# Kernel optimization log

Hardware: AMD Instinct MI355X
Metric: run time of the kernel (lower is better)

Reference implementation:

```python
import jax, jax.numpy as jnp
import numpy as np

T, B, C = 1024, 16, 1024
H, K, PAD_L = 16, 7, 3  # num_heads, kernel_size, padding_l
OUT = 1024


def setup_inputs() -> dict:
    key = jax.random.key(0)
    ks = jax.random.split(key, 8)
    s_in = 1.0 / np.sqrt(C)
    return {
        "x": jax.random.normal(ks[0], (T, B, C), dtype=jnp.float32),
        "W1": jax.random.normal(ks[1], (C, C), dtype=jnp.float32) * s_in,
        "b1": jnp.zeros((C,), dtype=jnp.float32),
        "Wq": jax.random.normal(ks[2], (C, H * K), dtype=jnp.float32) * s_in,
        "bq": jnp.zeros((H * K,), dtype=jnp.float32),
        "conv_bias": jax.random.normal(ks[3], (C,), dtype=jnp.float32) * 0.02,
        "W2": jax.random.normal(ks[4], (C, OUT), dtype=jnp.float32) * s_in,
        "b2": jnp.zeros((OUT,), dtype=jnp.float32),
    }


def reference(x, W1, b1, Wq, bq, conv_bias, W2, b2):
    # linear1 (glu=False -> no activation)
    h = x @ W1 + b1                       # [T, B, C]
    Tn, Bn, Cn = h.shape
    R = Cn // H                           # channels per head
    # dynamic filter prediction from query (= h), softmax over K taps
    w = (h @ Wq + bq).reshape(Tn, Bn, H, K)
    w = jax.nn.softmax(w, axis=-1)        # [T, B, H, K]
    # unfold1d: pad PAD_L left, K-1-PAD_L right along time, gather K-windows
    hp = jnp.pad(h, ((PAD_L, K - 1 - PAD_L), (0, 0), (0, 0)))
    win = jnp.stack([hp[k:k + Tn] for k in range(K)], axis=-1)  # [T, B, C, K]
    win = win.reshape(Tn, Bn, H, R, K)
    out = jnp.einsum('tbhrk,tbhk->tbhr', win, w).reshape(Tn, Bn, Cn)
    out = out + conv_bias                 # [T, B, C]
    return out @ W2 + b2                  # [T, B, OUT]
```

## Files before the change

kernel.cpp:

```cpp
#include <hip/hip_runtime.h>
#include <math.h>

#define T_DIM 1024
#define B_DIM 16
#define C_DIM 1024
#define H_DIM 16
#define K_TAPS 7
#define PAD_LEFT 3
#define OUT_DIM 1024
#define M_DIM (T_DIM * B_DIM)
#define HK 112
#define HKP 128
#define KD 1024
#define NT (KD / 64)

typedef __attribute__((ext_vector_type(8))) short bf16x8;
typedef __attribute__((ext_vector_type(4))) float f32x4;

__device__ __forceinline__ ushort f2bf(float f) {
    union { float f; unsigned u; } v; v.f = f;
    unsigned u = v.u;
    u += 0x7fffu + ((u >> 16) & 1u);
    return (ushort)(u >> 16);
}
__device__ __forceinline__ float bf2f(ushort h) {
    union { unsigned u; float f; } v; v.u = ((unsigned)h) << 16;
    return v.f;
}

__global__ __launch_bounds__(256) void cvt_bf16x8(const float* __restrict__ in,
                                                  ushort* __restrict__ out,
                                                  int n8) {
    int i = blockIdx.x * blockDim.x + threadIdx.x;
    if (i >= n8) return;
    const float4* p = (const float4*)in;
    float4 a = p[2 * i], b = p[2 * i + 1];
    uint4 o;
    o.x = (unsigned)f2bf(a.x) | ((unsigned)f2bf(a.y) << 16);
    o.y = (unsigned)f2bf(a.z) | ((unsigned)f2bf(a.w) << 16);
    o.z = (unsigned)f2bf(b.x) | ((unsigned)f2bf(b.y) << 16);
    o.w = (unsigned)f2bf(b.z) | ((unsigned)f2bf(b.w) << 16);
    ((uint4*)out)[i] = o;
}

__global__ void transpose_cvt(const float* __restrict__ W,
                              ushort* __restrict__ Wt,
                              int Kd, int N, int Npad) {
    __shared__ float tile[32][33];
    int n0 = blockIdx.x * 32, k0 = blockIdx.y * 32;
    int tx = threadIdx.x, ty = threadIdx.y;
#pragma unroll
    for (int j = 0; j < 4; ++j) {
        int k = k0 + ty * 4 + j;
        int n = n0 + tx;
        tile[ty * 4 + j][tx] = (n < N) ? W[(size_t)k * N + n] : 0.f;
    }
    __syncthreads();
#pragma unroll
    for (int j = 0; j < 4; ++j) {
        int n = n0 + ty * 4 + j;
        if (n < Npad)
            Wt[(size_t)n * Kd + k0 + tx] = f2bf(tile[tx][ty * 4 + j]);
    }
}

#define MFMA_HALF(AF, BF, MOFF)                                               \
    __builtin_amdgcn_s_setprio(1);                                            \
    _Pragma("unroll")                                                         \
    for (int m = 0; m < 4; ++m)                                               \
        _Pragma("unroll")                                                     \
        for (int n = 0; n < 4; ++n)                                           \
            acc[m + MOFF][n] = __builtin_amdgcn_mfma_f32_16x16x32_bf16(       \
                AF[m], BF[n], acc[m + MOFF][n], 0, 0, 0);                     \
    __builtin_amdgcn_s_setprio(0);

template <bool OUT_BF16>
__global__ __launch_bounds__(512, 2) void gemm256(
    const ushort* __restrict__ A, const ushort* __restrict__ Bt,
    const float* __restrict__ bias, void* __restrict__ Cp, int ldc) {
    __shared__ ushort Ab[2][256 * 64];
    __shared__ ushort Bb[2][256 * 64];

    const int tid  = threadIdx.x;
    const int lane = tid & 63;
    const int wid  = tid >> 6;
    const int wr = wid >> 2;
    const int wc = wid & 3;
    const int fr = lane & 15;
    const int fq = lane >> 4;

    const int orig = blockIdx.x;
    const int nid  = (orig & 7) * 32 + (orig >> 3);
    const int bm = (nid >> 2) * 256;
    const int bn = (nid & 3) * 256;

    const int r0  = tid >> 3;
    const int kb0 = ((tid & 7) ^ (r0 & 7)) * 8;
    const size_t srcA0 = (size_t)(bm + r0) * KD + kb0;
    const size_t srcB0 = (size_t)(bn + r0) * KD + kb0;

    const int swb = (fq * 8) ^ ((fr & 7) << 3);
    const int baseA0 = (wr * 128 + fr) * 64 + swb;
    const int baseB0 = (wc * 64 + fr) * 64 + swb;
    const int baseA1 = baseA0 ^ 32;
    const int baseB1 = baseB0 ^ 32;

    f32x4 acc[8][4];
#pragma unroll
    for (int m = 0; m < 8; ++m)
#pragma unroll
        for (int n = 0; n < 4; ++n) acc[m][n] = (f32x4){0.f, 0.f, 0.f, 0.f};

    auto stage = [&](int buf, int koff) {
        const ushort* Ap = A + srcA0 + koff;
        const ushort* Bp = Bt + srcB0 + koff;
#pragma unroll
        for (int i = 0; i < 4; ++i) {
            __builtin_amdgcn_global_load_lds(
                (const __attribute__((address_space(1))) void*)(Ap + (size_t)i * 64 * KD),
                (__attribute__((address_space(3))) void*)(&Ab[buf][(i * 512 + wid * 64) * 8]),
                16, 0, 0);
            __builtin_amdgcn_global_load_lds(
                (const __attribute__((address_space(1))) void*)(Bp + (size_t)i * 64 * KD),
                (__attribute__((address_space(3))) void*)(&Bb[buf][(i * 512 + wid * 64) * 8]),
                16, 0, 0);
        }
    };

    stage(0, 0);
    stage(1, 64);
    asm volatile("s_waitcnt vmcnt(8)" ::: "memory");
    __builtin_amdgcn_sched_barrier(0);
    __builtin_amdgcn_s_barrier();

#pragma unroll 1
    for (int t = 0; t < NT; ++t) {
        const int cur = t & 1;
        const ushort* Ac = &Ab[cur][0];
        const ushort* Bc = &Bb[cur][0];

        {
            bf16x8 b0[4], aA[4];
#pragma unroll
            for (int n = 0; n < 4; ++n)
                b0[n] = *(const bf16x8*)(Bc + baseB0 + n * 1024);
#pragma unroll
            for (int m = 0; m < 4; ++m)
                aA[m] = *(const bf16x8*)(Ac + baseA0 + m * 1024);
            MFMA_HALF(aA, b0, 0)
#pragma unroll
            for (int m = 0; m < 4; ++m)
                aA[m] = *(const bf16x8*)(Ac + baseA0 + (m + 4) * 1024);
            MFMA_HALF(aA, b0, 4)
        }

        bf16x8 b1[4], cB[4];
        {
            bf16x8 cA[4];
#pragma unroll
            for (int n = 0; n < 4; ++n)
                b1[n] = *(const bf16x8*)(Bc + baseB1 + n * 1024);
#pragma unroll
            for (int m = 0; m < 4; ++m)
                cA[m] = *(const bf16x8*)(Ac + baseA1 + m * 1024);
            MFMA_HALF(cA, b1, 0)
        }
#pragma unroll
        for (int m = 0; m < 4; ++m)
            cB[m] = *(const bf16x8*)(Ac + baseA1 + (m + 4) * 1024);

        if (t < NT - 1) {
            asm volatile("s_waitcnt lgkmcnt(0)" ::: "memory");
            __builtin_amdgcn_sched_barrier(0);
            __builtin_amdgcn_s_barrier();
            if (t < NT - 2) stage(cur, (t + 2) * 64);

            MFMA_HALF(cB, b1, 4)

            if (t < NT - 2) {
                asm volatile("s_waitcnt vmcnt(8)" ::: "memory");
            } else {
                asm volatile("s_waitcnt vmcnt(0)" ::: "memory");
            }
            __builtin_amdgcn_sched_barrier(0);
            __builtin_amdgcn_s_barrier();
        } else {
            MFMA_HALF(cB, b1, 4)
        }
    }

#pragma unroll
    for (int n = 0; n < 4; ++n) {
        int col = bn + wc * 64 + n * 16 + fr;
        float bv = bias[col];
#pragma unroll
        for (int m = 0; m < 8; ++m) {
#pragma unroll
            for (int r = 0; r < 4; ++r) {
                int row = bm + wr * 128 + m * 16 + fq * 4 + r;
                float v = acc[m][n][r] + bv;
                if (OUT_BF16)
                    ((ushort*)Cp)[(size_t)row * ldc + col] = f2bf(v);
                else
                    ((float*)Cp)[(size_t)row * ldc + col] = v;
            }
        }
    }
}

template <bool OUT_BF16, bool NGUARD>
__global__ __launch_bounds__(256) void gemm_mfma(const ushort* __restrict__ A,
                                                 const ushort* __restrict__ Bt,
                                                 const float* __restrict__ bias,
                                                 void* __restrict__ Cp,
                                                 int Kd, int N, int ldc) {
    __shared__ ushort Als[128 * 32];
    __shared__ ushort Bls[128 * 32];
    const int tid  = threadIdx.x;
    const int lane = tid & 63;
    const int wid  = tid >> 6;
    const int wr = wid >> 1, wc = wid & 1;
    const int bm = blockIdx.y * 128, bn = blockIdx.x * 128;
    const int fq = lane >> 4, fr = lane & 15;

    f32x4 acc[4][4];
#pragma unroll
    for (int m = 0; m < 4; ++m)
#pragma unroll
        for (int n = 0; n < 4; ++n) acc[m][n] = (f32x4){0.f, 0.f, 0.f, 0.f};

    const int c0 = wid * 128 + lane;
    const int c1 = c0 + 64;
    const int r0 = c0 >> 2, o0 = (c0 & 3) * 8;
    const int r1 = c1 >> 2, o1 = (c1 & 3) * 8;

    for (int k0 = 0; k0 < Kd; k0 += 32) {
        __builtin_amdgcn_global_load_lds(
            (const __attribute__((address_space(1))) void*)&A[(size_t)(bm + r0) * Kd + k0 + o0],
            (__attribute__((address_space(3))) void*)&Als[(wid * 2 + 0) * 512], 16, 0, 0);
        __builtin_amdgcn_global_load_lds(
            (const __attribute__((address_space(1))) void*)&A[(size_t)(bm + r1) * Kd + k0 + o1],
            (__attribute__((address_space(3))) void*)&Als[(wid * 2 + 1) * 512], 16, 0, 0);
        __builtin_amdgcn_global_load_lds(
            (const __attribute__((address_space(1))) void*)&Bt[(size_t)(bn + r0) * Kd + k0 + o0],
            (__attribute__((address_space(3))) void*)&Bls[(wid * 2 + 0) * 512], 16, 0, 0);
        __builtin_amdgcn_global_load_lds(
            (const __attribute__((address_space(1))) void*)&Bt[(size_t)(bn + r1) * Kd + k0 + o1],
            (__attribute__((address_space(3))) void*)&Bls[(wid * 2 + 1) * 512], 16, 0, 0);
        __syncthreads();

        bf16x8 af[4], bfr[4];
#pragma unroll
        for (int m = 0; m < 4; ++m)
            af[m] = *(const bf16x8*)&Als[(wr * 64 + m * 16 + fr) * 32 + fq * 8];
#pragma unroll
        for (int n = 0; n < 4; ++n)
            bfr[n] = *(const bf16x8*)&Bls[(wc * 64 + n * 16 + fr) * 32 + fq * 8];
#pragma unroll
        for (int m = 0; m < 4; ++m)
#pragma unroll
            for (int n = 0; n < 4; ++n)
                acc[m][n] = __builtin_amdgcn_mfma_f32_16x16x32_bf16(
                    af[m], bfr[n], acc[m][n], 0, 0, 0);
        __syncthreads();
    }

#pragma unroll
    for (int m = 0; m < 4; ++m) {
#pragma unroll
        for (int n = 0; n < 4; ++n) {
            int col = bn + wc * 64 + n * 16 + fr;
            if (NGUARD && col >= N) continue;
            float bv = bias[col];
#pragma unroll
            for (int r = 0; r < 4; ++r) {
                int row = bm + wr * 64 + m * 16 + fq * 4 + r;
                float v = acc[m][n][r] + bv;
                if (OUT_BF16)
                    ((ushort*)Cp)[(size_t)row * ldc + col] = f2bf(v);
                else
                    ((float*)Cp)[(size_t)row * ldc + col] = v;
            }
        }
    }
}

__global__ __launch_bounds__(256) void dynconv_bf16(const ushort* __restrict__ h,
                                                    const float* __restrict__ q,
                                                    const float* __restrict__ cbias,
                                                    ushort* __restrict__ out) {
    const int m = blockIdx.x;
    const int t = m >> 4;
    const int b = m & 15;

    __shared__ float wsm[HK];
    if (threadIdx.x < HK)
        wsm[threadIdx.x] = q[(size_t)m * HK + threadIdx.x];
    __syncthreads();
    if (threadIdx.x < H_DIM) {
        float* p = &wsm[threadIdx.x * K_TAPS];
        float mx = p[0];
#pragma unroll
        for (int k = 1; k < K_TAPS; ++k) mx = fmaxf(mx, p[k]);
        float e[K_TAPS], s = 0.f;
#pragma unroll
        for (int k = 0; k < K_TAPS; ++k) { e[k] = __expf(p[k] - mx); s += e[k]; }
        float inv = 1.f / s;
#pragma unroll
        for (int k = 0; k < K_TAPS; ++k) p[k] = e[k] * inv;
    }
    __syncthreads();

    const int c = threadIdx.x * 4;
    const int hh = c >> 6;

    float4 bias = *(const float4*)&cbias[c];
    float a0 = bias.x, a1 = bias.y, a2 = bias.z, a3 = bias.w;

#pragma unroll
    for (int k = 0; k < K_TAPS; ++k) {
        int tt = t + k - PAD_LEFT;
        if (tt < 0 || tt >= T_DIM) continue;
        ushort4 hv = *(const ushort4*)&h[((size_t)tt * B_DIM + b) * C_DIM + c];
        float wk = wsm[hh * K_TAPS + k];
        a0 = fmaf(bf2f(hv.x), wk, a0);
        a1 = fmaf(bf2f(hv.y), wk, a1);
        a2 = fmaf(bf2f(hv.z), wk, a2);
        a3 = fmaf(bf2f(hv.w), wk, a3);
    }
    ushort4 o;
    o.x = f2bf(a0); o.y = f2bf(a1); o.z = f2bf(a2); o.w = f2bf(a3);
    *(ushort4*)&out[(size_t)m * C_DIM + c] = o;
}

extern "C" void kernel_launch(void* const* d_in, const int* in_sizes, int n_in,
                              void* d_out, int out_size, void* d_ws,
                              size_t ws_size, hipStream_t stream) {
    const float* x     = (const float*)d_in[0];
    const float* W1    = (const float*)d_in[1];
    const float* b1    = (const float*)d_in[2];
    const float* Wq    = (const float*)d_in[3];
    const float* bq    = (const float*)d_in[4];
    const float* cbias = (const float*)d_in[5];
    const float* W2    = (const float*)d_in[6];
    const float* b2    = (const float*)d_in[7];
    float* out = (float*)d_out;

    ushort* xb    = (ushort*)d_ws;
    ushort* hb    = xb    + (size_t)M_DIM * C_DIM;
    ushort* convb = hb    + (size_t)M_DIM * C_DIM;
    ushort* W1t   = convb + (size_t)M_DIM * C_DIM;
    ushort* W2t   = W1t   + (size_t)C_DIM * C_DIM;
    ushort* Wqt   = W2t   + (size_t)C_DIM * OUT_DIM;
    float*  q     = (float*)(Wqt + (size_t)HKP * C_DIM);

    cvt_bf16x8<<<dim3(M_DIM * C_DIM / 8 / 256), dim3(256), 0, stream>>>(
        x, xb, M_DIM * C_DIM / 8);
    transpose_cvt<<<dim3(C_DIM / 32, C_DIM / 32), dim3(32, 8), 0, stream>>>(
        W1, W1t, C_DIM, C_DIM, C_DIM);
    transpose_cvt<<<dim3(HKP / 32, C_DIM / 32), dim3(32, 8), 0, stream>>>(
        Wq, Wqt, C_DIM, HK, HKP);
    transpose_cvt<<<dim3(OUT_DIM / 32, C_DIM / 32), dim3(32, 8), 0, stream>>>(
        W2, W2t, C_DIM, OUT_DIM, OUT_DIM);

    gemm256<true><<<dim3(256), dim3(512), 0, stream>>>(xb, W1t, b1, hb, C_DIM);

    gemm_mfma<false, true>
        <<<dim3(1, M_DIM / 128), dim3(256), 0, stream>>>(
            hb, Wqt, bq, q, C_DIM, HK, HK);

    dynconv_bf16<<<dim3(M_DIM), dim3(256), 0, stream>>>(hb, q, cbias, convb);

    gemm256<false><<<dim3(256), dim3(512), 0, stream>>>(convb, W2t, b2, out,
                                                        OUT_DIM);
}
```

Measured before the change: 162.6 us.

## Replace 256x256 K64 GEMM with 256x128 K32 tile using four-wave blocks

The big GEMM kernel is rewritten from a 256x256 tile with K-step 64 and 8 waves to a 256x128 tile with K-step 32 and 4 waves per block, launched as 512 blocks. The LDS swizzle is removed, the split half-step MFMA schedule is simplified to a single load-then-MFMA loop per K32 step, and the block remap is adjusted. This aims to shrink LDS and register footprint, raise occupancy, and reduce schedule complexity. In exchange it lowers arithmetic intensity per block, doubles the number of barriers, and unswizzled LDS reads may hit bank conflicts.

```diff
diff --git a/kernel.cpp b/kernel.cpp
--- a/kernel.cpp
+++ b/kernel.cpp
@@ -12,7 +12,7 @@
 #define HK 112
 #define HKP 128
 #define KD 1024
-#define NT (KD / 64)
+#define NT32 (KD / 32)
 
 typedef __attribute__((ext_vector_type(8))) short bf16x8;
 typedef __attribute__((ext_vector_type(4))) float f32x4;
@@ -64,46 +64,33 @@
     }
 }
 
-#define MFMA_HALF(AF, BF, MOFF)                                               \
-    __builtin_amdgcn_s_setprio(1);                                            \
-    _Pragma("unroll")                                                         \
-    for (int m = 0; m < 4; ++m)                                               \
-        _Pragma("unroll")                                                     \
-        for (int n = 0; n < 4; ++n)                                           \
-            acc[m + MOFF][n] = __builtin_amdgcn_mfma_f32_16x16x32_bf16(       \
-                AF[m], BF[n], acc[m + MOFF][n], 0, 0, 0);                     \
-    __builtin_amdgcn_s_setprio(0);
-
 template <bool OUT_BF16>
-__global__ __launch_bounds__(512, 2) void gemm256(
+__global__ __launch_bounds__(256, 2) void gemm_k32(
     const ushort* __restrict__ A, const ushort* __restrict__ Bt,
     const float* __restrict__ bias, void* __restrict__ Cp, int ldc) {
-    __shared__ ushort Ab[2][256 * 64];
-    __shared__ ushort Bb[2][256 * 64];
+    __shared__ ushort Ab[2][256 * 32];
+    __shared__ ushort Bb[2][128 * 32];
 
     const int tid  = threadIdx.x;
     const int lane = tid & 63;
     const int wid  = tid >> 6;
-    const int wr = wid >> 2;
-    const int wc = wid & 3;
+    const int wr = wid >> 1;
+    const int wc = wid & 1;
     const int fr = lane & 15;
     const int fq = lane >> 4;
 
     const int orig = blockIdx.x;
-    const int nid  = (orig & 7) * 32 + (orig >> 3);
-    const int bm = (nid >> 2) * 256;
-    const int bn = (nid & 3) * 256;
-
-    const int r0  = tid >> 3;
-    const int kb0 = ((tid & 7) ^ (r0 & 7)) * 8;
-    const size_t srcA0 = (size_t)(bm + r0) * KD + kb0;
-    const size_t srcB0 = (size_t)(bn + r0) * KD + kb0;
-
-    const int swb = (fq * 8) ^ ((fr & 7) << 3);
-    const int baseA0 = (wr * 128 + fr) * 64 + swb;
-    const int baseB0 = (wc * 64 + fr) * 64 + swb;
-    const int baseA1 = baseA0 ^ 32;
-    const int baseB1 = baseB0 ^ 32;
+    const int nid  = (orig & 7) * 64 + (orig >> 3);
+    const int bm = (nid >> 3) * 256;
+    const int bn = (nid & 7) * 128;
+
+    const int rA   = tid >> 2;
+    const int slA  = (tid & 3) * 8;
+    const size_t srcA0 = (size_t)(bm + rA) * KD + slA;
+    const size_t srcB0 = (size_t)(bn + rA) * KD + slA;
+
+    const int aBase0 = (wr * 128 + fr) * 32 + fq * 8;
+    const int bBase0 = (wc * 64 + fr) * 32 + fq * 8;
 
     f32x4 acc[8][4];
 #pragma unroll
@@ -111,82 +98,65 @@
 #pragma unroll
         for (int n = 0; n < 4; ++n) acc[m][n] = (f32x4){0.f, 0.f, 0.f, 0.f};
 
-    auto stage = [&](int buf, int koff) {
-        const ushort* Ap = A + srcA0 + koff;
-        const ushort* Bp = Bt + srcB0 + koff;
-#pragma unroll
-        for (int i = 0; i < 4; ++i) {
+    auto stage = [&](int buf, int t) {
+        const ushort* Ap = A + srcA0 + t * 32;
+        const ushort* Bp = Bt + srcB0 + t * 32;
+#pragma unroll
+        for (int i = 0; i < 4; ++i)
             __builtin_amdgcn_global_load_lds(
                 (const __attribute__((address_space(1))) void*)(Ap + (size_t)i * 64 * KD),
-                (__attribute__((address_space(3))) void*)(&Ab[buf][(i * 512 + wid * 64) * 8]),
+                (__attribute__((address_space(3))) void*)(&Ab[buf][(i * 256 + wid * 64) * 8]),
                 16, 0, 0);
+#pragma unroll
+        for (int i = 0; i < 2; ++i)
             __builtin_amdgcn_global_load_lds(
                 (const __attribute__((address_space(1))) void*)(Bp + (size_t)i * 64 * KD),
-                (__attribute__((address_space(3))) void*)(&Bb[buf][(i * 512 + wid * 64) * 8]),
+                (__attribute__((address_space(3))) void*)(&Bb[buf][(i * 256 + wid * 64) * 8]),
                 16, 0, 0);
-        }
     };
 
     stage(0, 0);
-    stage(1, 64);
-    asm volatile("s_waitcnt vmcnt(8)" ::: "memory");
+    stage(1, 1);
+    asm volatile("s_waitcnt vmcnt(6)" ::: "memory");
     __builtin_amdgcn_sched_barrier(0);
     __builtin_amdgcn_s_barrier();
 
 #pragma unroll 1
-    for (int t = 0; t < NT; ++t) {
+    for (int t = 0; t < NT32; ++t) {
         const int cur = t & 1;
         const ushort* Ac = &Ab[cur][0];
         const ushort* Bc = &Bb[cur][0];
 
-        {
-            bf16x8 b0[4], aA[4];
+        bf16x8 a[8], b[4];
+#pragma unroll
+        for (int n = 0; n < 4; ++n)
+            b[n] = *(const bf16x8*)(Bc + bBase0 + n * 512);
+#pragma unroll
+        for (int m = 0; m < 8; ++m)
+            a[m] = *(const bf16x8*)(Ac + aBase0 + m * 512);
+
+        asm volatile("s_waitcnt lgkmcnt(0)" ::: "memory");
+        __builtin_amdgcn_sched_barrier(0);
+        __builtin_amdgcn_s_barrier();
+
+        if (t < NT32 - 2) stage(cur, t + 2);
+
+        __builtin_amdgcn_s_setprio(1);
+#pragma unroll
+        for (int m = 0; m < 8; ++m)
 #pragma unroll
             for (int n = 0; n < 4; ++n)
-                b0[n] = *(const bf16x8*)(Bc + baseB0 + n * 1024);
-#pragma unroll
-            for (int m = 0; m < 4; ++m)
-                aA[m] = *(const bf16x8*)(Ac + baseA0 + m * 1024);
-            MFMA_HALF(aA, b0, 0)
-#pragma unroll
-            for (int m = 0; m < 4; ++m)
-                aA[m] = *(const bf16x8*)(Ac + baseA0 + (m + 4) * 1024);
-            MFMA_HALF(aA, b0, 4)
+                acc[m][n] = __builtin_amdgcn_mfma_f32_16x16x32_bf16(
+                    a[m], b[n], acc[m][n], 0, 0, 0);
+        __builtin_amdgcn_s_setprio(0);
+
+        if (t < NT32 - 2) {
+            asm volatile("s_waitcnt vmcnt(6)" ::: "memory");
+        } else if (t == NT32 - 2) {
+            asm volatile("s_waitcnt vmcnt(0)" ::: "memory");
         }
-
-        bf16x8 b1[4], cB[4];
-        {
-            bf16x8 cA[4];
-#pragma unroll
-            for (int n = 0; n < 4; ++n)
-                b1[n] = *(const bf16x8*)(Bc + baseB1 + n * 1024);
-#pragma unroll
-            for (int m = 0; m < 4; ++m)
-                cA[m] = *(const bf16x8*)(Ac + baseA1 + m * 1024);
-            MFMA_HALF(cA, b1, 0)
-        }
-#pragma unroll
-        for (int m = 0; m < 4; ++m)
-            cB[m] = *(const bf16x8*)(Ac + baseA1 + (m + 4) * 1024);
-
-        if (t < NT - 1) {
-            asm volatile("s_waitcnt lgkmcnt(0)" ::: "memory");
-            __builtin_amdgcn_sched_barrier(0);
-            __builtin_amdgcn_s_barrier();
-            if (t < NT - 2) stage(cur, (t + 2) * 64);
-
-            MFMA_HALF(cB, b1, 4)
-
-            if (t < NT - 2) {
-                asm volatile("s_waitcnt vmcnt(8)" ::: "memory");
-            } else {
-                asm volatile("s_waitcnt vmcnt(0)" ::: "memory");
-            }
-            __builtin_amdgcn_sched_barrier(0);
-            __builtin_amdgcn_s_barrier();
-        } else {
-            MFMA_HALF(cB, b1, 4)
-        }
+        __builtin_amdgcn_sched_barrier(0);
+        if (t < NT32 - 1) __builtin_amdgcn_s_barrier();
     }
 
 #pragma unroll
@@ -363,7 +333,7 @@
     transpose_cvt<<<dim3(OUT_DIM / 32, C_DIM / 32), dim3(32, 8), 0, stream>>>(
         W2, W2t, C_DIM, OUT_DIM, OUT_DIM);
 
-    gemm256<true><<<dim3(256), dim3(512), 0, stream>>>(xb, W1t, b1, hb, C_DIM);
+    gemm_k32<true><<<dim3(512), dim3(256), 0, stream>>>(xb, W1t, b1, hb, C_DIM);
 
     gemm_mfma<false, true>
         <<<dim3(1, M_DIM / 128), dim3(256), 0, stream>>>(
@@ -371,6 +341,6 @@
 
     dynconv_bf16<<<dim3(M_DIM), dim3(256), 0, stream>>>(hb, q, cbias, convb);
 
-    gemm256<false><<<dim3(256), dim3(512), 0, stream>>>(convb, W2t, b2, out,
-                                                        OUT_DIM);
-}
+    gemm_k32<false><<<dim3(512), dim3(256), 0, stream>>>(convb, W2t, b2, out,
+                                                         OUT_DIM);
+}
```

New measurement: 171.7 us. 5.6% more time.
